# Kernel optimization log

Hardware: AMD Instinct MI355X
Metric: run time of the kernel (lower is better)

Reference implementation:

```python
import jax, jax.numpy as jnp
import numpy as np

B, NV, JN = 1024, 8, 21
V = NV * JN            # 168 tokens = num_view * joint_num
F_DIM, NH, DQ, DV = 512, 4, 128, 128
HID = 512
EPS = 1e-6
NEG = float(-2**32 + 1)


def _layer_norm(x, g, b):
    mu = jnp.mean(x, axis=-1, keepdims=True)
    var = jnp.mean(jnp.square(x - mu), axis=-1, keepdims=True)
    return (x - mu) * jax.lax.rsqrt(var + EPS) * g + b


def setup_inputs() -> dict:
    key = jax.random.key(0)
    ks = jax.random.split(key, 12)
    s = 0.02
    return {
        "x": jax.random.normal(ks[0], (B, V, F_DIM), dtype=jnp.float32),
        "valid": jax.random.randint(ks[1], (B, NV), 0, 2),
        "wq": jax.random.normal(ks[2], (NH * DQ, F_DIM), dtype=jnp.float32) * s,
        "bq": jnp.zeros((NH * DQ,), dtype=jnp.float32),
        "wk": jax.random.normal(ks[3], (NH * DQ, F_DIM), dtype=jnp.float32) * s,
        "bk": jnp.zeros((NH * DQ,), dtype=jnp.float32),
        "wv": jax.random.normal(ks[4], (NH * DV, F_DIM), dtype=jnp.float32) * s,
        "bv": jnp.zeros((NH * DV,), dtype=jnp.float32),
        "fc_w": jax.random.normal(ks[5], (F_DIM, NH * DV), dtype=jnp.float32) * s,
        "fc_b": jnp.zeros((F_DIM,), dtype=jnp.float32),
        "ln1_g": jnp.ones((F_DIM,), dtype=jnp.float32),
        "ln1_b": jnp.zeros((F_DIM,), dtype=jnp.float32),
        "ln2_g": jnp.ones((F_DIM,), dtype=jnp.float32),
        "ln2_b": jnp.zeros((F_DIM,), dtype=jnp.float32),
        "fc1_w": jax.random.normal(ks[6], (HID, F_DIM), dtype=jnp.float32) * s,
        "fc1_b": jnp.zeros((HID,), dtype=jnp.float32),
        "fc2_w": jax.random.normal(ks[7], (F_DIM, HID), dtype=jnp.float32) * s,
        "fc2_b": jnp.zeros((F_DIM,), dtype=jnp.float32),
    }


def reference(x, valid, wq, bq, wk, bk, wv, bv, fc_w, fc_b,
              ln1_g, ln1_b, ln2_g, ln2_b, fc1_w, fc1_b, fc2_w, fc2_b):
    bs = x.shape[0]
    h = _layer_norm(x, ln1_g, ln1_b)                          # [B,V,f]
    q = (h @ wq.T + bq).reshape(bs, V, NH, DQ)                # [B,V,H,dq]
    k = (h @ wk.T + bk).reshape(bs, V, NH, DQ)
    v = (h @ wv.T + bv).reshape(bs, V, NH, DV)
    attn = jnp.einsum('bqhd,bkhd->bhqk', q, k) / jnp.sqrt(jnp.float32(DQ))
    # valid mask: per-view validity expanded to per-token, pairwise additive
    w = jnp.where(valid == 0, NEG, 0.0).astype(x.dtype)       # [B,NV]
    w = jnp.repeat(w, JN, axis=1)                             # [B,V], view-major
    m = w[:, :, None] + w[:, None, :]                         # [B,V,V]
    attn = attn + m[:, None, :, :]
    attn = jax.nn.softmax(attn, axis=-1)
    out = jnp.einsum('bhqk,bkhd->bqhd', attn, v).reshape(bs, V, NH * DV)
    out = out @ fc_w.T + fc_b
    x = x + out
    # MLP residual block
    h2 = _layer_norm(x, ln2_g, ln2_b)
    h2 = jax.nn.relu(h2 @ fc1_w.T + fc1_b) @ fc2_w.T + fc2_b
    return x + h2
```

## Files before the change

### kernel.cpp

```cpp
#include <hip/hip_runtime.h>
#include <stdint.h>

#define BATCH 1024
#define NVIEW 8
#define JN_   21
#define VTOK  168
#define FDIM  512
#define NHEAD 4
#define DHEAD 128
#define MROWS (BATCH*VTOK)
#define SCALE2 0.127517434f

typedef __attribute__((ext_vector_type(8))) short s8v;
typedef __attribute__((ext_vector_type(4))) short s4v;
typedef __attribute__((ext_vector_type(4))) float f4v;

static __device__ __forceinline__ short f2bf(float f){
  unsigned u = __builtin_bit_cast(unsigned, f);
  unsigned r = (u + 0x7FFFu + ((u >> 16) & 1u)) >> 16;
  return (short)(unsigned short)r;
}
static __device__ __forceinline__ float bf2f(short s){
  unsigned u = ((unsigned)(unsigned short)s) << 16;
  return __builtin_bit_cast(float, u);
}

#define GL16(gp, lp) __builtin_amdgcn_global_load_lds( \
    (__attribute__((address_space(1))) void*)(gp), \
    (__attribute__((address_space(3))) void*)(lp), 16, 0, 0)

__global__ __launch_bounds__(256) void convert_w(
    const float* __restrict__ wq, const float* __restrict__ wk,
    const float* __restrict__ wv, const float* __restrict__ fcw,
    const float* __restrict__ fc1, const float* __restrict__ fc2,
    short* __restrict__ dst){
  int id = blockIdx.x * 256 + threadIdx.x;
  int e = id * 4;
  int seg = e >> 18;
  int off = e & 262143;
  const float* s = seg==0?wq: seg==1?wk: seg==2?wv: seg==3?fcw: seg==4?fc1: fc2;
  float4 u = *(const float4*)(s + off);
  s4v o; o[0]=f2bf(u.x); o[1]=f2bf(u.y); o[2]=f2bf(u.z); o[3]=f2bf(u.w);
  *(s4v*)(dst + e) = o;
}

__global__ __launch_bounds__(256) void ln1_kernel(
    const float* __restrict__ x, const float* __restrict__ g,
    const float* __restrict__ bb, short* __restrict__ h){
  int row  = blockIdx.x * 4 + (threadIdx.x >> 6);
  int lane = threadIdx.x & 63;
  size_t base = (size_t)row * 512 + lane * 8;
  float4 u0 = *(const float4*)(x + base);
  float4 u1 = *(const float4*)(x + base + 4);
  float s = u0.x+u0.y+u0.z+u0.w + u1.x+u1.y+u1.z+u1.w;
  float q = u0.x*u0.x+u0.y*u0.y+u0.z*u0.z+u0.w*u0.w
          + u1.x*u1.x+u1.y*u1.y+u1.z*u1.z+u1.w*u1.w;
  #pragma unroll
  for (int o = 1; o < 64; o <<= 1){ s += __shfl_xor(s,o); q += __shfl_xor(q,o); }
  float mu = s * (1.f/512.f);
  float rstd = rsqrtf(q*(1.f/512.f) - mu*mu + 1e-6f);
  float4 g0 = *(const float4*)(g + lane*8),  g1 = *(const float4*)(g + lane*8 + 4);
  float4 b0 = *(const float4*)(bb + lane*8), b1 = *(const float4*)(bb + lane*8 + 4);
  s8v o_;
  o_[0]=f2bf((u0.x-mu)*rstd*g0.x+b0.x); o_[1]=f2bf((u0.y-mu)*rstd*g0.y+b0.y);
  o_[2]=f2bf((u0.z-mu)*rstd*g0.z+b0.z); o_[3]=f2bf((u0.w-mu)*rstd*g0.w+b0.w);
  o_[4]=f2bf((u1.x-mu)*rstd*g1.x+b1.x); o_[5]=f2bf((u1.y-mu)*rstd*g1.y+b1.y);
  o_[6]=f2bf((u1.z-mu)*rstd*g1.z+b1.z); o_[7]=f2bf((u1.w-mu)*rstd*g1.w+b1.w);
  *(s8v*)(h + base) = o_;
}

__global__ __launch_bounds__(256) void ln2_kernel(
    const short* __restrict__ x2b, const float* __restrict__ g,
    const float* __restrict__ bb, short* __restrict__ g2){
  int row  = blockIdx.x * 4 + (threadIdx.x >> 6);
  int lane = threadIdx.x & 63;
  size_t base = (size_t)row * 512 + lane * 8;
  s8v xv = *(const s8v*)(x2b + base);
  float v[8];
  #pragma unroll
  for (int i = 0; i < 8; i++) v[i] = bf2f(xv[i]);
  float s = 0.f, q = 0.f;
  #pragma unroll
  for (int i = 0; i < 8; i++){ s += v[i]; q += v[i]*v[i]; }
  #pragma unroll
  for (int o = 1; o < 64; o <<= 1){ s += __shfl_xor(s,o); q += __shfl_xor(q,o); }
  float mu = s * (1.f/512.f);
  float rstd = rsqrtf(q*(1.f/512.f) - mu*mu + 1e-6f);
  float4 g0 = *(const float4*)(g + lane*8),  g1 = *(const float4*)(g + lane*8 + 4);
  float4 b0 = *(const float4*)(bb + lane*8), b1 = *(const float4*)(bb + lane*8 + 4);
  s8v o_;
  o_[0]=f2bf((v[0]-mu)*rstd*g0.x+b0.x); o_[1]=f2bf((v[1]-mu)*rstd*g0.y+b0.y);
  o_[2]=f2bf((v[2]-mu)*rstd*g0.z+b0.z); o_[3]=f2bf((v[3]-mu)*rstd*g0.w+b0.w);
  o_[4]=f2bf((v[4]-mu)*rstd*g1.x+b1.x); o_[5]=f2bf((v[5]-mu)*rstd*g1.y+b1.y);
  o_[6]=f2bf((v[6]-mu)*rstd*g1.z+b1.z); o_[7]=f2bf((v[7]-mu)*rstd*g1.w+b1.w);
  *(s8v*)(g2 + base) = o_;
}

template<int MODE>
__global__ __launch_bounds__(512, 1) void gemm_bt(
    const short* __restrict__ A, const short* __restrict__ Bm,
    const float* __restrict__ bias0, const float* __restrict__ bias1,
    const short* __restrict__ aux, const float* __restrict__ auxf,
    short* __restrict__ out0, short* __restrict__ out1,
    float* __restrict__ outf){
  __shared__ short lds[81920];
  short* const AL = lds;
  short* const BL = lds + 49152;
  const int tid = threadIdx.x, lane = tid & 63;
  const int wid = tid >> 6, wr = wid >> 2, wc = wid & 3;
  const int lg = lane >> 4, l15 = lane & 15, l7 = lane & 7;
  const int nwg  = gridDim.x * gridDim.y;
  const int flat = blockIdx.y * gridDim.x + blockIdx.x;
  const int swz  = (flat & 7) * (nwg >> 3) + (flat >> 3);
  size_t mt, nt;
  if (MODE == 1){ mt = swz & 1; nt = (size_t)(swz >> 1); }
  else {
    constexpr int GX = (MODE == 0) ? 4 : 2;
    nt = swz % GX; mt = swz / GX;
  }
  const size_t m0 = mt * 256, n0 = nt * 256;
  const short* Ab = A + m0 * 512;
  const short* Bb = Bm + n0 * 512;

#define STAGEA(slot, tile, half) do {                                   \
    const short* s_ = Ab + (size_t)(half)*65536 + (tile)*64;            \
    short* d_ = AL + (slot)*8192;                                       \
    _Pragma("unroll")                                                   \
    for (int r_ = 0; r_ < 2; r_++){                                     \
      int c_ = r_*512 + tid;                                            \
      int row_ = c_ >> 3, chk_ = (c_ & 7) ^ (row_ & 7);                 \
      GL16(s_ + (size_t)row_*512 + chk_*8, d_ + c_*8);                  \
    } } while(0)
#define STAGEB(slot, tile, half) do {                                   \
    const short* s_ = Bb + (size_t)(half)*65536 + (tile)*64;            \
    short* d_ = BL + (slot)*8192;                                       \
    _Pragma("unroll")                                                   \
    for (int r_ = 0; r_ < 2; r_++){                                     \
      int c_ = r_*512 + tid;                                            \
      int row_ = c_ >> 3, chk_ = (c_ & 7) ^ (row_ & 7);                 \
      GL16(s_ + (size_t)row_*512 + chk_*8, d_ + c_*8);                  \
    } } while(0)

  STAGEA(0, 0, 0); STAGEA(1, 0, 1);
  STAGEB(0, 0, 0); STAGEB(1, 0, 1);
  STAGEA(2, 1, 0); STAGEA(3, 1, 1);
  asm volatile("s_waitcnt vmcnt(4)" ::: "memory");
  __builtin_amdgcn_s_barrier();

  f4v acc[8][4];
  #pragma unroll
  for (int m=0;m<8;m++)
    #pragma unroll
    for (int n=0;n<4;n++) acc[m][n] = f4v{0.f,0.f,0.f,0.f};

  s8v a0[8], b0[4];
  #pragma unroll
  for (int t = 0; t < 8; ++t){
    const short* Awp = AL + ((2*t)%6 + wr)*8192 + l15*64;
    const short* Bwp = BL + ((2*t)%4 + (wc>>1))*8192 + ((wc&1)*64 + l15)*64;
    const int c0 = (lg ^ l7) * 8;
    const int c1 = ((4 + lg) ^ l7) * 8;
    #pragma unroll
    for (int n=0;n<4;n++) b0[n] = *(const s8v*)(Bwp + n*1024 + c0);
    #pragma unroll
    for (int m=0;m<8;m++) a0[m] = *(const s8v*)(Awp + m*1024 + c0);
    if (t < 7){ STAGEB((2*t+2)%4, t+1, 0); STAGEB((2*t+2)%4 + 1, t+1, 1); }
    __builtin_amdgcn_s_setprio(1);
    #pragma unroll
    for (int m=0;m<8;m++)
      #pragma unroll
      for (int n=0;n<4;n++)
        acc[m][n] = __builtin_amdgcn_mfma_f32_16x16x32_bf16(a0[m], b0[n], acc[m][n], 0,0,0);
    __builtin_amdgcn_s_setprio(0);
    #pragma unroll
    for (int n=0;n<4;n++) b0[n] = *(const s8v*)(Bwp + n*1024 + c1);
    #pragma unroll
    for (int m=0;m<8;m++) a0[m] = *(const s8v*)(Awp + m*1024 + c1);
    if (t < 6){ STAGEA((2*t+4)%6, t+2, 0); STAGEA((2*t+4)%6 + 1, t+2, 1); }
    __builtin_amdgcn_s_setprio(1);
    #pragma unroll
    for (int m=0;m<8;m++)
      #pragma unroll
      for (int n=0;n<4;n++)
        acc[m][n] = __builtin_amdgcn_mfma_f32_16x16x32_bf16(a0[m], b0[n], acc[m][n], 0,0,0);
    __builtin_amdgcn_s_setprio(0);
    if (t < 6)       asm volatile("s_waitcnt vmcnt(4)" ::: "memory");
    else if (t == 6) asm volatile("s_waitcnt vmcnt(0)" ::: "memory");
    __builtin_amdgcn_s_barrier();
  }
#undef STAGEA
#undef STAGEB

  #pragma unroll
  for (int m=0;m<8;m++)
  #pragma unroll
  for (int n=0;n<4;n++)
  #pragma unroll
  for (int r=0;r<4;r++){
    int rowL = wr*128 + m*16 + lg*4 + r;
    int colL = wc*64 + n*16 + l15;
    size_t gm = m0 + rowL, gn = n0 + colL;
    float val = acc[m][n][r];
    if (MODE == 0){
      int nn = (int)gn;
      val += (nn < 512) ? bias0[nn] : bias1[nn - 512];
      int head = (nn >> 7) & 3, d = nn & 127;
      size_t b = gm / 168, tok = gm - b * 168;
      size_t idx = ((b*4 + head)*168 + tok)*128 + d;
      ((nn < 512) ? out0 : out1)[idx] = f2bf(val);
    } else if (MODE == 1){
      val += bias0[gm];
      int hh = ((int)gm >> 7) & 3, d = (int)gm & 127;
      size_t b = gn / 168, tok = gn - b * 168;
      out0[((b*4 + hh)*128 + d)*168 + tok] = f2bf(val);
    } else if (MODE == 2){
      val += bias0[gn] + auxf[gm*512 + gn];
      out0[gm*512 + gn] = f2bf(val);
    } else if (MODE == 3){
      val += bias0[gn];
      val = fmaxf(val, 0.f);
      out0[gm*512 + gn] = f2bf(val);
    } else {
      val += bias0[gn] + bf2f(aux[gm*512 + gn]);
      outf[gm*512 + gn] = val;
    }
  }
}

__global__ __launch_bounds__(256, 2) void attn_kernel(
    const short* __restrict__ qg_, const short* __restrict__ kg_,
    const short* __restrict__ vtg_, const int* __restrict__ valid,
    short* __restrict__ outp){
  __shared__ short ldsb[38400];
  short* const Kl = ldsb;
  short* const Ps = ldsb;

  int tid = threadIdx.x, lane = tid & 63, wid = tid >> 6;
  int lg = lane >> 4, l15 = lane & 15;
  int bh = blockIdx.x, b = bh >> 2, hh = bh & 3;
  const short* qg  = qg_  + (size_t)bh * (168*128);
  const short* kg  = kg_  + (size_t)bh * (168*128);
  const short* vtg = vtg_ + (size_t)bh * (128*168);

  #pragma unroll
  for (int r = 0; r < 11; r++){
    int c = r*256 + tid;
    int row = c >> 4;
    int g = (c & 15) ^ ((row & 1) << 2);
    GL16(kg + (size_t)row*128 + g*8, Kl + c*8);
  }

  int bits = 0;
  #pragma unroll
  for (int v = 0; v < 8; v++) bits |= (valid[b*8 + v] != 0) << v;
  if (bits == 0) bits = 255;
  float wk2[11];
  #pragma unroll
  for (int n = 0; n < 11; n++){
    int kt = n*16 + l15;
    int view = (kt * 781) >> 14;
    wk2[n] = ((bits >> view) & 1) ? 0.0f : -1.0e9f;
  }

  int row0 = wid * 48;
  f4v zf = {0.f,0.f,0.f,0.f};

  s8v qf[3][4];
  #pragma unroll
  for (int m=0;m<3;m++)
    #pragma unroll
    for (int kf=0;kf<4;kf++)
      qf[m][kf] = *(const s8v*)(qg + (size_t)(row0 + m*16 + l15)*128 + kf*32 + lg*8);

  asm volatile("s_waitcnt vmcnt(0)" ::: "memory");
  __builtin_amdgcn_s_barrier();

  f4v accS[3][11];
  #pragma unroll
  for (int m=0;m<3;m++)
    #pragma unroll
    for (int n=0;n<11;n++) accS[m][n] = zf;
  #pragma unroll
  for (int n=0;n<11;n++){
    s8v kb[4];
    #pragma unroll
    for (int kf=0;kf<4;kf++)
      kb[kf] = *(const s8v*)&Kl[(size_t)(n*16 + l15)*128 + (((kf*4 + lg) ^ ((l15 & 1) << 2)) << 3)];
    __builtin_amdgcn_s_setprio(1);
    #pragma unroll
    for (int kf=0;kf<4;kf++)
      #pragma unroll
      for (int m=0;m<3;m++)
        accS[m][n] = __builtin_amdgcn_mfma_f32_16x16x32_bf16(qf[m][kf], kb[kf], accS[m][n], 0,0,0);
    __builtin_amdgcn_s_setprio(0);
  }
  __builtin_amdgcn_s_barrier();

  s8v vb[3][6];
  #pragma unroll
  for (int p=0;p<2;p++)
    #pragma unroll
    for (int kf=0;kf<6;kf++)
      vb[p][kf] = *(const s8v*)(vtg + (size_t)(p*16 + l15)*168 + kf*32 + lg*8);

  float inv_[3][4];
  #pragma unroll
  for (int m=0;m<3;m++){
    #pragma unroll
    for (int r=0;r<4;r++){
      int qtok = row0 + m*16 + lg*4 + r;
      float sum = 0.f;
      #pragma unroll
      for (int n=0;n<11;n++){
        float p = exp2f(fmaf(accS[m][n][r], SCALE2, wk2[n]));
        sum += p;
        Ps[qtok*200 + n*16 + l15] = f2bf(p);
      }
      sum += __shfl_xor(sum,1); sum += __shfl_xor(sum,2);
      sum += __shfl_xor(sum,4); sum += __shfl_xor(sum,8);
      inv_[m][r] = 1.0f / sum;
    }
  }
  {
    s8v z8 = {0,0,0,0,0,0,0,0};
    for (int i = lane; i < 96; i += 64){
      int rr = row0 + (i >> 1);
      *(s8v*)&Ps[rr*200 + 176 + (i&1)*8] = z8;
    }
  }

  s8v ap[3][6];
  #pragma unroll
  for (int m=0;m<3;m++)
    #pragma unroll
    for (int kf=0;kf<6;kf++)
      ap[m][kf] = *(const s8v*)&Ps[(row0 + m*16 + l15)*200 + kf*32 + lg*8];

  f4v accO[3][8];
  #pragma unroll
  for (int m=0;m<3;m++)
    #pragma unroll
    for (int n=0;n<8;n++) accO[m][n] = zf;
  #pragma unroll
  for (int n=0;n<8;n++){
    if (n < 6){
      #pragma unroll
      for (int kf=0;kf<6;kf++)
        vb[(n+2)%3][kf] = *(const s8v*)(vtg + (size_t)((n+2)*16 + l15)*168 + kf*32 + lg*8);
    }
    __builtin_amdgcn_s_setprio(1);
    #pragma unroll
    for (int kf=0;kf<6;kf++)
      #pragma unroll
      for (int m=0;m<3;m++)
        accO[m][n] = __builtin_amdgcn_mfma_f32_16x16x32_bf16(ap[m][kf], vb[n%3][kf], accO[m][n], 0,0,0);
    __builtin_amdgcn_s_setprio(0);
  }

  #pragma unroll
  for (int m=0;m<3;m++){
    #pragma unroll
    for (int r=0;r<4;r++){
      int qtok = row0 + m*16 + lg*4 + r;
      if (qtok < 168){
        float iv = inv_[m][r];
        size_t base = ((size_t)b*168 + qtok)*512 + hh*128;
        #pragma unroll
        for (int n=0;n<8;n++)
          outp[base + n*16 + l15] = f2bf(accO[m][n][r] * iv);
      }
    }
  }
}

extern "C" void kernel_launch(void* const* d_in, const int* in_sizes, int n_in,
                              void* d_out, int out_size, void* d_ws, size_t ws_size,
                              hipStream_t stream) {
  const float* x     = (const float*)d_in[0];
  const int*   valid = (const int*)  d_in[1];
  const float* wq    = (const float*)d_in[2];
  const float* bq    = (const float*)d_in[3];
  const float* wk    = (const float*)d_in[4];
  const float* bk    = (const float*)d_in[5];
  const float* wv    = (const float*)d_in[6];
  const float* bv    = (const float*)d_in[7];
  const float* fcw   = (const float*)d_in[8];
  const float* fcb   = (const float*)d_in[9];
  const float* ln1g  = (const float*)d_in[10];
  const float* ln1b  = (const float*)d_in[11];
  const float* ln2g  = (const float*)d_in[12];
  const float* ln2b  = (const float*)d_in[13];
  const float* fc1w  = (const float*)d_in[14];
  const float* fc1b  = (const float*)d_in[15];
  const float* fc2w  = (const float*)d_in[16];
  const float* fc2b  = (const float*)d_in[17];

  char* ws = (char*)d_ws;
  short* h       = (short*)(ws + 0LL);
  short* q_ws    = (short*)(ws + 176160768LL);
  short* k_ws    = (short*)(ws + 352321536LL);
  short* vt_ws   = (short*)(ws + 528482304LL);
  short* wb      = (short*)(ws + 704643072LL);
  short* attn_o  = h;
  short* g2      = h;
  short* a1      = k_ws;
  short* x2b     = vt_ws;
  float* outp    = (float*)d_out;

  convert_w<<<1536, 256, 0, stream>>>(wq, wk, wv, fcw, fc1w, fc2w, wb);
  ln1_kernel<<<MROWS/4, 256, 0, stream>>>(x, ln1g, ln1b, h);
  gemm_bt<0><<<dim3(4, MROWS/256), 512, 0, stream>>>(h, wb, bq, bk, nullptr, nullptr, q_ws, k_ws, nullptr);
  gemm_bt<1><<<dim3(2, MROWS/256), 512, 0, stream>>>(wb + 524288, h, bv, nullptr, nullptr, nullptr, vt_ws, nullptr, nullptr);
  attn_kernel<<<BATCH*NHEAD, 256, 0, stream>>>(q_ws, k_ws, vt_ws, valid, attn_o);
  gemm_bt<2><<<dim3(2, MROWS/256), 512, 0, stream>>>(attn_o, wb + 786432, fcb, nullptr, nullptr, x, x2b, nullptr, nullptr);
  ln2_kernel<<<MROWS/4, 256, 0, stream>>>(x2b, ln2g, ln2b, g2);
  gemm_bt<3><<<dim3(2, MROWS/256), 512, 0, stream>>>(g2, wb + 1048576, fc1b, nullptr, nullptr, nullptr, a1, nullptr, nullptr);
  gemm_bt<4><<<dim3(2, MROWS/256), 512, 0, stream>>>(a1, wb + 1310720, fc2b, nullptr, x2b, nullptr, nullptr, nullptr, outp);
}
```

Before: 1.225 ms.

## Make GEMM kernel persistent with cross-tile continuous prefetch pipeline

Turns gemm_bt into a persistent kernel with 256 workgroups that walk output tiles in a strided order. The K-loop becomes one continuous stage counter across tiles, so loads for the next tile are issued while the current tile finishes, and the epilogue runs every eighth stage. This removes the pipeline fill and drain at each tile boundary and the block launch overhead. In exchange the loop is no longer fully unrolled (runtime slot indices), the epilogue stores sit inside the main loop, and the tile swizzle that grouped blocks for L2 reuse is gone.

Result: slower. 1.593 ms (+30.0%).

```diff
diff --git a/kernel.cpp b/kernel.cpp
--- a/kernel.cpp
+++ b/kernel.cpp
@@ -109,41 +109,43 @@
   const int tid = threadIdx.x, lane = tid & 63;
   const int wid = tid >> 6, wr = wid >> 2, wc = wid & 3;
   const int lg = lane >> 4, l15 = lane & 15, l7 = lane & 7;
-  const int nwg  = gridDim.x * gridDim.y;
-  const int flat = blockIdx.y * gridDim.x + blockIdx.x;
-  const int swz  = (flat & 7) * (nwg >> 3) + (flat >> 3);
-  size_t mt, nt;
-  if (MODE == 1){ mt = swz & 1; nt = (size_t)(swz >> 1); }
-  else {
-    constexpr int GX = (MODE == 0) ? 4 : 2;
-    nt = swz % GX; mt = swz / GX;
-  }
-  const size_t m0 = mt * 256, n0 = nt * 256;
-  const short* Ab = A + m0 * 512;
-  const short* Bb = Bm + n0 * 512;
-
-#define STAGEA(slot, tile, half) do {                                   \
-    const short* s_ = Ab + (size_t)(half)*65536 + (tile)*64;            \
-    short* d_ = AL + (slot)*8192;                                       \
-    _Pragma("unroll")                                                   \
-    for (int r_ = 0; r_ < 2; r_++){                                     \
-      int c_ = r_*512 + tid;                                            \
-      int row_ = c_ >> 3, chk_ = (c_ & 7) ^ (row_ & 7);                 \
-      GL16(s_ + (size_t)row_*512 + chk_*8, d_ + c_*8);                  \
-    } } while(0)
-#define STAGEB(slot, tile, half) do {                                   \
-    const short* s_ = Bb + (size_t)(half)*65536 + (tile)*64;            \
-    short* d_ = BL + (slot)*8192;                                       \
-    _Pragma("unroll")                                                   \
-    for (int r_ = 0; r_ < 2; r_++){                                     \
-      int c_ = r_*512 + tid;                                            \
-      int row_ = c_ >> 3, chk_ = (c_ & 7) ^ (row_ & 7);                 \
-      GL16(s_ + (size_t)row_*512 + chk_*8, d_ + c_*8);                  \
-    } } while(0)
-
-  STAGEA(0, 0, 0); STAGEA(1, 0, 1);
-  STAGEB(0, 0, 0); STAGEB(1, 0, 1);
-  STAGEA(2, 1, 0); STAGEA(3, 1, 1);
+  const int bid = blockIdx.x;
+  constexpr int NT = (MODE == 0) ? 2688 : 1344;
+  const int Send = ((NT - bid + 255) >> 8) << 3;
+
+#define MTOF(it) ((MODE==0) ? ((it)>>2) : (MODE==1 ? ((it)&1) : ((it)>>1)))
+#define NTOF(it) ((MODE==0) ? ((it)&3) : (MODE==1 ? ((it)>>1) : ((it)&1)))
+
+#define STAGEAS(s, slot) do {                                             \
+    int it_ = bid + (((s) >> 3) << 8);                                    \
+    const short* sb_ = A + (size_t)MTOF(it_)*131072 + (size_t)((s)&7)*64; \
+    short* d_ = AL + (slot)*8192;                                         \
+    _Pragma("unroll")                                                     \
+    for (int h_ = 0; h_ < 2; h_++)                                        \
+      _Pragma("unroll")                                                   \
+      for (int r_ = 0; r_ < 2; r_++){                                     \
+        int c_ = r_*512 + tid;                                            \
+        int row_ = c_ >> 3, chk_ = (c_ & 7) ^ (row_ & 7);                 \
+        GL16(sb_ + (size_t)h_*65536 + (size_t)row_*512 + chk_*8,          \
+             d_ + h_*8192 + c_*8);                                        \
+      } } while(0)
+#define STAGEBS(s, slot) do {                                             \
+    int it_ = bid + (((s) >> 3) << 8);                                    \
+    const short* sb_ = Bm + (size_t)NTOF(it_)*131072 + (size_t)((s)&7)*64;\
+    short* d_ = BL + (slot)*8192;                                         \
+    _Pragma("unroll")                                                     \
+    for (int h_ = 0; h_ < 2; h_++)                                        \
+      _Pragma("unroll")                                                   \
+      for (int r_ = 0; r_ < 2; r_++){                                     \
+        int c_ = r_*512 + tid;                                            \
+        int row_ = c_ >> 3, chk_ = (c_ & 7) ^ (row_ & 7);                 \
+        GL16(sb_ + (size_t)h_*65536 + (size_t)row_*512 + chk_*8,          \
+             d_ + h_*8192 + c_*8);                                        \
+      } } while(0)
+
+  STAGEAS(0, 0);
+  STAGEBS(0, 0);
+  STAGEAS(1, 2);
   asm volatile("s_waitcnt vmcnt(4)" ::: "memory");
   __builtin_amdgcn_s_barrier();
 
@@ -153,18 +155,18 @@
     #pragma unroll
     for (int n=0;n<4;n++) acc[m][n] = f4v{0.f,0.f,0.f,0.f};
 
+  int slotA = 0, slotB = 0;
   s8v a0[8], b0[4];
-  #pragma unroll
-  for (int t = 0; t < 8; ++t){
-    const short* Awp = AL + ((2*t)%6 + wr)*8192 + l15*64;
-    const short* Bwp = BL + ((2*t)%4 + (wc>>1))*8192 + ((wc&1)*64 + l15)*64;
+  for (int s = 0; s < Send; ++s){
+    const short* Awp = AL + (slotA + wr)*8192 + l15*64;
+    const short* Bwp = BL + (slotB + (wc>>1))*8192 + ((wc&1)*64 + l15)*64;
     const int c0 = (lg ^ l7) * 8;
     const int c1 = ((4 + lg) ^ l7) * 8;
     #pragma unroll
     for (int n=0;n<4;n++) b0[n] = *(const s8v*)(Bwp + n*1024 + c0);
     #pragma unroll
     for (int m=0;m<8;m++) a0[m] = *(const s8v*)(Awp + m*1024 + c0);
-    if (t < 7){ STAGEB((2*t+2)%4, t+1, 0); STAGEB((2*t+2)%4 + 1, t+1, 1); }
+    if (s + 1 < Send) STAGEBS(s+1, slotB ^ 2);
     __builtin_amdgcn_s_setprio(1);
     #pragma unroll
     for (int m=0;m<8;m++)
@@ -176,7 +178,7 @@
     for (int n=0;n<4;n++) b0[n] = *(const s8v*)(Bwp + n*1024 + c1);
     #pragma unroll
     for (int m=0;m<8;m++) a0[m] = *(const s8v*)(Awp + m*1024 + c1);
-    if (t < 6){ STAGEA((2*t+4)%6, t+2, 0); STAGEA((2*t+4)%6 + 1, t+2, 1); }
+    if (s + 2 < Send) STAGEAS(s+2, (slotA >= 2) ? slotA - 2 : slotA + 4);
     __builtin_amdgcn_s_setprio(1);
     #pragma unroll
     for (int m=0;m<8;m++)
@@ -184,47 +186,58 @@
       for (int n=0;n<4;n++)
         acc[m][n] = __builtin_amdgcn_mfma_f32_16x16x32_bf16(a0[m], b0[n], acc[m][n], 0,0,0);
     __builtin_amdgcn_s_setprio(0);
-    if (t < 6)       asm volatile("s_waitcnt vmcnt(4)" ::: "memory");
-    else if (t == 6) asm volatile("s_waitcnt vmcnt(0)" ::: "memory");
+    if (s + 2 < Send)       asm volatile("s_waitcnt vmcnt(4)" ::: "memory");
+    else if (s + 2 == Send) asm volatile("s_waitcnt vmcnt(0)" ::: "memory");
     __builtin_amdgcn_s_barrier();
-  }
-#undef STAGEA
-#undef STAGEB
-
-  #pragma unroll
-  for (int m=0;m<8;m++)
-  #pragma unroll
-  for (int n=0;n<4;n++)
-  #pragma unroll
-  for (int r=0;r<4;r++){
-    int rowL = wr*128 + m*16 + lg*4 + r;
-    int colL = wc*64 + n*16 + l15;
-    size_t gm = m0 + rowL, gn = n0 + colL;
-    float val = acc[m][n][r];
-    if (MODE == 0){
-      int nn = (int)gn;
-      val += (nn < 512) ? bias0[nn] : bias1[nn - 512];
-      int head = (nn >> 7) & 3, d = nn & 127;
-      size_t b = gm / 168, tok = gm - b * 168;
-      size_t idx = ((b*4 + head)*168 + tok)*128 + d;
-      ((nn < 512) ? out0 : out1)[idx] = f2bf(val);
-    } else if (MODE == 1){
-      val += bias0[gm];
-      int hh = ((int)gm >> 7) & 3, d = (int)gm & 127;
-      size_t b = gn / 168, tok = gn - b * 168;
-      out0[((b*4 + hh)*128 + d)*168 + tok] = f2bf(val);
-    } else if (MODE == 2){
-      val += bias0[gn] + auxf[gm*512 + gn];
-      out0[gm*512 + gn] = f2bf(val);
-    } else if (MODE == 3){
-      val += bias0[gn];
-      val = fmaxf(val, 0.f);
-      out0[gm*512 + gn] = f2bf(val);
-    } else {
-      val += bias0[gn] + bf2f(aux[gm*512 + gn]);
-      outf[gm*512 + gn] = val;
+    if ((s & 7) == 7){
+      const int it_ = bid + ((s >> 3) << 8);
+      const size_t m0 = (size_t)MTOF(it_) * 256, n0 = (size_t)NTOF(it_) * 256;
+      #pragma unroll
+      for (int m=0;m<8;m++)
+      #pragma unroll
+      for (int n=0;n<4;n++)
+      #pragma unroll
+      for (int r=0;r<4;r++){
+        int rowL = wr*128 + m*16 + lg*4 + r;
+        int colL = wc*64 + n*16 + l15;
+        size_t gm = m0 + rowL, gn = n0 + colL;
+        float val = acc[m][n][r];
+        if (MODE == 0){
+          int nn = (int)gn;
+          val += (nn < 512) ? bias0[nn] : bias1[nn - 512];
+          int head = (nn >> 7) & 3, d = nn & 127;
+          size_t b = gm / 168, tok = gm - b * 168;
+          size_t idx = ((b*4 + head)*168 + tok)*128 + d;
+          ((nn < 512) ? out0 : out1)[idx] = f2bf(val);
+        } else if (MODE == 1){
+          val += bias0[gm];
+          int hh = ((int)gm >> 7) & 3, d = (int)gm & 127;
+          size_t b = gn / 168, tok = gn - b * 168;
+          out0[((b*4 + hh)*128 + d)*168 + tok] = f2bf(val);
+        } else if (MODE == 2){
+          val += bias0[gn] + auxf[gm*512 + gn];
+          out0[gm*512 + gn] = f2bf(val);
+        } else if (MODE == 3){
+          val += bias0[gn];
+          val = fmaxf(val, 0.f);
+          out0[gm*512 + gn] = f2bf(val);
+        } else {
+          val += bias0[gn] + bf2f(aux[gm*512 + gn]);
+          outf[gm*512 + gn] = val;
+        }
+      }
+      #pragma unroll
+      for (int m=0;m<8;m++)
+        #pragma unroll
+        for (int n=0;n<4;n++) acc[m][n] = f4v{0.f,0.f,0.f,0.f};
     }
-  }
+    slotA = (slotA >= 4) ? 0 : slotA + 2;
+    slotB ^= 2;
+  }
+#undef STAGEAS
+#undef STAGEBS
+#undef MTOF
+#undef NTOF
 }
 
 __global__ __launch_bounds__(256, 2) void attn_kernel(
@@ -409,11 +422,11 @@
 
   convert_w<<<1536, 256, 0, stream>>>(wq, wk, wv, fcw, fc1w, fc2w, wb);
   ln1_kernel<<<MROWS/4, 256, 0, stream>>>(x, ln1g, ln1b, h);
-  gemm_bt<0><<<dim3(4, MROWS/256), 512, 0, stream>>>(h, wb, bq, bk, nullptr, nullptr, q_ws, k_ws, nullptr);
-  gemm_bt<1><<<dim3(2, MROWS/256), 512, 0, stream>>>(wb + 524288, h, bv, nullptr, nullptr, nullptr, vt_ws, nullptr, nullptr);
+  gemm_bt<0><<<256, 512, 0, stream>>>(h, wb, bq, bk, nullptr, nullptr, q_ws, k_ws, nullptr);
+  gemm_bt<1><<<256, 512, 0, stream>>>(wb + 524288, h, bv, nullptr, nullptr, nullptr, vt_ws, nullptr, nullptr);
   attn_kernel<<<BATCH*NHEAD, 256, 0, stream>>>(q_ws, k_ws, vt_ws, valid, attn_o);
-  gemm_bt<2><<<dim3(2, MROWS/256), 512, 0, stream>>>(attn_o, wb + 786432, fcb, nullptr, nullptr, x, x2b, nullptr, nullptr);
+  gemm_bt<2><<<256, 512, 0, stream>>>(attn_o, wb + 786432, fcb, nullptr, nullptr, x, x2b, nullptr, nullptr);
   ln2_kernel<<<MROWS/4, 256, 0, stream>>>(x2b, ln2g, ln2b, g2);
-  gemm_bt<3><<<dim3(2, MROWS/256), 512, 0, stream>>>(g2, wb + 1048576, fc1b, nullptr, nullptr, nullptr, a1, nullptr, nullptr);
-  gemm_bt<4><<<dim3(2, MROWS/256), 512, 0, stream>>>(a1, wb + 1310720, fc2b, nullptr, x2b, nullptr, nullptr, nullptr, outp);
-}
+  gemm_bt<3><<<256, 512, 0, stream>>>(g2, wb + 1048576, fc1b, nullptr, nullptr, nullptr, a1, nullptr, nullptr);
+  gemm_bt<4><<<256, 512, 0, stream>>>(a1, wb + 1310720, fc2b, nullptr, x2b, nullptr, nullptr, nullptr, outp);
+}
```
